# Performance work log

Hardware: AMD Instinct MI355X
Metric: run time of the kernel (lower is better)

The kernel has to match this reference:

```python
import jax, jax.numpy as jnp
import numpy as np

NH = 8       # attention_maps
DK = 256     # key_dimension
DV = 256     # value_dimension
KS = 3       # kernel_size
PAD = (KS - 1) // 2


def _conv(x, w, b, stride, pad):
    y = jax.lax.conv_general_dilated(
        x, w, (stride, stride), [(pad, pad), (pad, pad)],
        dimension_numbers=('NCHW', 'OIHW', 'NCHW'))
    return y + b[None, :, None, None]


def _rel_to_abs(x):
    # x: (B, M, L, 2L-1) -> (B, M, L, L) via the skewing/padding trick
    B, M, L, _ = x.shape
    x = jnp.pad(x, ((0, 0), (0, 0), (0, 0), (0, 1)))          # (B,M,L,2L)
    x = x.reshape(B, M, 2 * L * L)
    x = jnp.pad(x, ((0, 0), (0, 0), (0, L - 1)))
    x = x.reshape(B, M, L + 1, 2 * L - 1)
    return x[:, :, :L, L - 1:]


def _rel_logits_1d(q, kr, H, W, nh, axis):
    # q: (B, nh, H, W, dkh); kr: (2W-1, dkh)
    B = q.shape[0]
    rl = jnp.einsum('bhxyd,md->bhxym', q, kr)                 # (B,nh,H,W,2W-1)
    rl = rl.reshape(B, nh * H, W, 2 * W - 1)
    rl = _rel_to_abs(rl).reshape(B, nh, H, W, W)
    rl = jnp.broadcast_to(rl[:, :, :, None], (B, nh, H, H, W, W))
    if axis == 'x':
        rl = jnp.transpose(rl, (0, 1, 2, 4, 3, 5))
    else:
        # faithful to original torch code (incl. its no-op transpose bug):
        # transpose(4,5) then transpose(3,5) == permutation (0,1,2,4,5,3)
        rl = jnp.transpose(rl, (0, 1, 2, 4, 5, 3))
    return rl.reshape(B, nh, H * W, H * W)


def setup_inputs() -> dict:
    key = jax.random.key(0)
    ks = jax.random.split(key, 10)
    B, Cin, H, W = 4, 128, 32, 32
    Cout = 512
    dkh = DK // NH
    sc = 0.05
    return {
        'x': jax.random.normal(ks[0], (B, Cin, H, W), jnp.float32),
        'conv_w': jax.random.normal(ks[1], (Cout - DV, Cin, KS, KS), jnp.float32) * sc,
        'conv_b': jax.random.normal(ks[2], (Cout - DV,), jnp.float32) * sc,
        'qkv_w': jax.random.normal(ks[3], (2 * DK + DV, Cin, KS, KS), jnp.float32) * sc,
        'qkv_b': jax.random.normal(ks[4], (2 * DK + DV,), jnp.float32) * sc,
        'att_w': jax.random.normal(ks[5], (DV, DV, 1, 1), jnp.float32) * sc,
        'att_b': jax.random.normal(ks[6], (DV,), jnp.float32) * sc,
        'kr_x': jax.random.normal(ks[7], (2 * W - 1, dkh), jnp.float32),
        'kr_y': jax.random.normal(ks[8], (2 * H - 1, dkh), jnp.float32),
    }


def reference(x, conv_w, conv_b, qkv_w, qkv_b, att_w, att_b, kr_x, kr_y):
    B = x.shape[0]
    conv_out = _conv(x, conv_w, conv_b, 1, PAD)               # (B, Cout-DV, H, W)
    H, W = conv_out.shape[2], conv_out.shape[3]
    dkh, dvh = DK // NH, DV // NH

    qkv = _conv(x, qkv_w, qkv_b, 1, PAD)                      # (B, 2DK+DV, H, W)
    q, k, v = jnp.split(qkv, [DK, 2 * DK], axis=1)
    q = q.reshape(B, NH, dkh, H, W) * (dkh ** -0.5)
    k = k.reshape(B, NH, dkh, H, W)
    v = v.reshape(B, NH, dvh, H, W)

    fq = q.reshape(B, NH, dkh, H * W)
    fk = k.reshape(B, NH, dkh, H * W)
    fv = v.reshape(B, NH, dvh, H * W)

    logits = jnp.einsum('bhdi,bhdj->bhij', fq, fk)            # (B,NH,HW,HW)

    # relative logits (scaled q, matching torch which scales before this)
    q_t = jnp.transpose(q, (0, 1, 3, 4, 2))                   # (B,NH,H,W,dkh)
    rel_x = _rel_logits_1d(q_t, kr_x, H, W, NH, 'x')
    rel_y = _rel_logits_1d(jnp.transpose(q_t, (0, 1, 3, 2, 4)), kr_y, W, H, NH, 'y')
    logits = logits + rel_y + rel_x

    weights = jax.nn.softmax(logits, axis=-1)
    att = jnp.einsum('bhij,bhdj->bhid', weights, fv)          # (B,NH,HW,dvh)
    # faithful raw reshape as in torch (no transpose before reshape)
    att = att.reshape(B, NH, dvh, H, W).reshape(B, DV, H, W)
    att = _conv(att, att_w, att_b, 1, 0)
    return jnp.concatenate([conv_out, att], axis=1)
```

## Files before the change

kernel.cpp:

```cpp
#include <hip/hip_runtime.h>
#include <hip/hip_bf16.h>
#include <math.h>

#define BN 4
#define CIN 128
#define HH 32
#define WW 32
#define HWP 1024
#define NHEAD 8

typedef __attribute__((ext_vector_type(8))) short s8v;
typedef __attribute__((ext_vector_type(4))) float f32x4;

__global__ __launch_bounds__(256) void prep_all(
    const float* __restrict__ x,
    const float* __restrict__ conv_w, const float* __restrict__ qkv_w,
    const float* __restrict__ att_w,
    const float* __restrict__ kr_x, const float* __restrict__ kr_y,
    __hip_bfloat16* __restrict__ xT, __hip_bfloat16* __restrict__ Wb,
    __hip_bfloat16* __restrict__ Wab, __hip_bfloat16* __restrict__ krb)
{
    const int bid = blockIdx.x;
    const int tid = threadIdx.x;

    if (bid < 4608) {
        int g = bid * 256 + tid;
        int co = g / 1152;
        int k = g - co * 1152;
        int kk = k >> 7, ci = k & 127;
        float v;
        if (co < 256) v = conv_w[((size_t)(co * 128 + ci) * 9) + kk];
        else          v = qkv_w[((size_t)((co - 256) * 128 + ci) * 9) + kk];
        Wb[(size_t)co * 1152 + k] = __float2bfloat16(v);
    } else if (bid < 4744) {
        __shared__ float xs[CIN][33];
        int rel = bid - 4608;
        int yy = rel >> 2;
        int b = rel & 3;
        const bool inner = (yy >= 1 && yy <= 32);
        if (inner) {
            for (int idx = tid; idx < CIN * 32; idx += 256) {
                int ci = idx >> 5, xx = idx & 31;
                xs[ci][xx] = x[((size_t)(b * CIN + ci) * HH + (yy - 1)) * WW + xx];
            }
        }
        __syncthreads();
        for (int idx = tid; idx < 34 * 128; idx += 256) {
            int xx = idx >> 7, ci = idx & 127;
            float v = 0.f;
            if (inner && xx >= 1 && xx <= 32) v = xs[ci][xx - 1];
            xT[((size_t)(b * 34 + yy) * 34 + xx) * 128 + ci] = __float2bfloat16(v);
        }
    } else if (bid < 5000) {
        int g = (bid - 4744) * 256 + tid;
        Wab[g] = __float2bfloat16(att_w[g]);
    } else {
        for (int idx = tid; idx < 2 * 64 * 32; idx += 256) {
            int axis = idx >> 11;
            int col = (idx >> 5) & 63;
            int d = idx & 31;
            float v = 0.f;
            if (col < 63) v = axis ? kr_y[col * 32 + d] : kr_x[col * 32 + d];
            krb[idx] = __float2bfloat16(v);
        }
    }
}

__global__ __launch_bounds__(256) void conv_gemm(
    const __hip_bfloat16* __restrict__ Wb, const __hip_bfloat16* __restrict__ xT,
    const float* __restrict__ conv_b, const float* __restrict__ qkv_b,
    float* __restrict__ out,
    __hip_bfloat16* __restrict__ qbf, __hip_bfloat16* __restrict__ kbf,
    __hip_bfloat16* __restrict__ vtb)
{
    __shared__ __align__(16) __hip_bfloat16 As[128 * 128];
    __shared__ __align__(16) __hip_bfloat16 Bs[128 * 128];

    const int tid = threadIdx.x;
    const int wv = tid >> 6;
    const int lane = tid & 63;
    const int n16 = lane & 15;
    const int quad = lane >> 4;
    const int co0 = blockIdx.x * 128;
    const int y0 = blockIdx.y * 4;
    const int b = blockIdx.z;
    const int mh = wv >> 1, nh = wv & 1;

    const int rbase = tid >> 4;
    const int hh = tid & 15;
    const int swz = (hh ^ rbase) * 8;
    const __hip_bfloat16* aGbase = Wb + (size_t)(co0 + rbase) * 1152 + hh * 8;

    f32x4 acc[4][4];
#pragma unroll
    for (int i = 0; i < 4; ++i)
#pragma unroll
        for (int j = 0; j < 4; ++j) acc[i][j] = (f32x4){0.f, 0.f, 0.f, 0.f};

    s8v ra[8], rb[8];

    auto load_tile = [&](int kk, s8v* la, s8v* lb) {
        const int ky = kk / 3, kx = kk - ky * 3;
#pragma unroll
        for (int i = 0; i < 8; ++i)
            la[i] = *reinterpret_cast<const s8v*>(aGbase + (size_t)(16 * i) * 1152 + kk * 128);
#pragma unroll
        for (int i = 0; i < 8; ++i) {
            int p = rbase + 16 * i;
            int row = y0 + (p >> 5) + ky;
            int xx = (p & 31) + kx;
            lb[i] = *reinterpret_cast<const s8v*>(
                xT + ((size_t)(b * 34 + row) * 34 + xx) * 128 + hh * 8);
        }
    };

    load_tile(0, ra, rb);

    for (int s = 0; s < 9; ++s) {
        __syncthreads();
#pragma unroll
        for (int i = 0; i < 8; ++i) {
            *reinterpret_cast<s8v*>(&As[(rbase + 16 * i) * 128 + swz]) = ra[i];
            *reinterpret_cast<s8v*>(&Bs[(rbase + 16 * i) * 128 + swz]) = rb[i];
        }
        __syncthreads();
        if (s < 8) load_tile(s + 1, ra, rb);

#pragma unroll
        for (int ksub = 0; ksub < 4; ++ksub) {
            const int chunk = ((ksub * 4 + quad) ^ n16) * 8;
            s8v af[4], bfr[4];
#pragma unroll
            for (int mt = 0; mt < 4; ++mt)
                af[mt] = *reinterpret_cast<const s8v*>(&As[(mh * 64 + mt * 16 + n16) * 128 + chunk]);
#pragma unroll
            for (int nt = 0; nt < 4; ++nt)
                bfr[nt] = *reinterpret_cast<const s8v*>(&Bs[(nh * 64 + nt * 16 + n16) * 128 + chunk]);
#pragma unroll
            for (int mt = 0; mt < 4; ++mt)
#pragma unroll
                for (int nt = 0; nt < 4; ++nt)
                    acc[mt][nt] = __builtin_amdgcn_mfma_f32_16x16x32_bf16(af[mt], bfr[nt], acc[mt][nt], 0, 0, 0);
        }
    }

    const int coBase = co0 + mh * 64;
    const int pixBase = y0 * 32 + nh * 64;
    const int seg = coBase >> 8;

    if (seg == 0) {
#pragma unroll
        for (int mt = 0; mt < 4; ++mt)
#pragma unroll
            for (int r = 0; r < 4; ++r) {
                int co = coBase + mt * 16 + quad * 4 + r;
                float bias = conv_b[co];
                float* op = out + (size_t)(b * 512 + co) * HWP + pixBase;
#pragma unroll
                for (int nt = 0; nt < 4; ++nt)
                    op[nt * 16 + n16] = acc[mt][nt][r] + bias;
            }
    } else if (seg == 1) {
        const float scale = 0.17677669529663687f;
#pragma unroll
        for (int mt = 0; mt < 4; ++mt)
#pragma unroll
            for (int r = 0; r < 4; ++r) {
                int c2 = coBase - 256 + mt * 16 + quad * 4 + r;
                float bias = qkv_b[c2];
                int h = c2 >> 5, d = c2 & 31;
                int bh = b * NHEAD + h;
#pragma unroll
                for (int nt = 0; nt < 4; ++nt) {
                    int pix = pixBase + nt * 16 + n16;
                    qbf[((size_t)bh * HWP + pix) * 32 + d] =
                        __float2bfloat16((acc[mt][nt][r] + bias) * scale);
                }
            }
    } else if (seg == 2) {
#pragma unroll
        for (int mt = 0; mt < 4; ++mt)
#pragma unroll
            for (int r = 0; r < 4; ++r) {
                int c2 = coBase - 512 + mt * 16 + quad * 4 + r;
                float bias = qkv_b[c2 + 256];
                int h = c2 >> 5, d = c2 & 31;
                int bh = b * NHEAD + h;
#pragma unroll
                for (int nt = 0; nt < 4; ++nt) {
                    int pix = pixBase + nt * 16 + n16;
                    kbf[((size_t)bh * HWP + pix) * 32 + d] =
                        __float2bfloat16(acc[mt][nt][r] + bias);
                }
            }
    } else {
#pragma unroll
        for (int mt = 0; mt < 4; ++mt)
#pragma unroll
            for (int r = 0; r < 4; ++r) {
                int c2 = coBase - 768 + mt * 16 + quad * 4 + r;
                float bias = qkv_b[c2 + 512];
                int h = c2 >> 5, d = c2 & 31;
                int bh = b * NHEAD + h;
                __hip_bfloat16* vp = vtb + ((size_t)bh * 32 + d) * HWP + pixBase;
#pragma unroll
                for (int nt = 0; nt < 4; ++nt)
                    vp[nt * 16 + n16] = __float2bfloat16(acc[mt][nt][r] + bias);
            }
    }
}

__global__ __launch_bounds__(256) void attn_kernel(
    const __hip_bfloat16* __restrict__ qbf, const __hip_bfloat16* __restrict__ kbf,
    const __hip_bfloat16* __restrict__ vtb, const __hip_bfloat16* __restrict__ krb,
    __hip_bfloat16* __restrict__ attc)
{
    __shared__ __align__(16) float QrX[4][16][68];
    __shared__ __align__(16) float QrY[4][16][68];
    __shared__ __align__(16) __hip_bfloat16 Pb[4][16][40];

    const int tid = threadIdx.x;
    const int wv = tid >> 6;
    const int lane = tid & 63;
    const int n16 = lane & 15;
    const int quad = lane >> 4;
    const int bh = blockIdx.x;
    const int i0 = (blockIdx.y * 4 + wv) * 16;
    const int xi0 = i0 & 31;
    const int yi0 = i0 >> 5;

    s8v aq = *reinterpret_cast<const s8v*>(
        qbf + ((size_t)bh * HWP + i0 + n16) * 32 + quad * 8);
    s8v aqT = *reinterpret_cast<const s8v*>(
        qbf + ((size_t)bh * HWP + (xi0 + n16) * 32 + yi0) * 32 + quad * 8);

#pragma unroll
    for (int t = 0; t < 4; ++t) {
        s8v bx = *reinterpret_cast<const s8v*>(krb + ((size_t)(t * 16 + n16)) * 32 + quad * 8);
        s8v by = *reinterpret_cast<const s8v*>(krb + ((size_t)(64 + t * 16 + n16)) * 32 + quad * 8);
        f32x4 cx = {0.f, 0.f, 0.f, 0.f}, cy = {0.f, 0.f, 0.f, 0.f};
        cx = __builtin_amdgcn_mfma_f32_16x16x32_bf16(aq, bx, cx, 0, 0, 0);
        cy = __builtin_amdgcn_mfma_f32_16x16x32_bf16(aqT, by, cy, 0, 0, 0);
#pragma unroll
        for (int r = 0; r < 4; ++r) {
            QrX[wv][quad * 4 + r][t * 16 + n16] = cx[r];
            QrY[wv][quad * 4 + r][t * 16 + n16] = cy[r];
        }
    }

    float rx0[4], rx1[4];
    int rybase[4];
#pragma unroll
    for (int r = 0; r < 4; ++r) {
        int xi = xi0 + quad * 4 + r;
        rx0[r] = QrX[wv][quad * 4 + r][n16 + 31 - xi];
        rx1[r] = QrX[wv][quad * 4 + r][n16 + 47 - xi];
        rybase[r] = 31 - xi;
    }

    float lsum[4] = {0.f, 0.f, 0.f, 0.f};
    f32x4 O0 = {0.f, 0.f, 0.f, 0.f}, O1 = {0.f, 0.f, 0.f, 0.f};

    const __hip_bfloat16* kbase = kbf + (size_t)bh * HWP * 32;
    const __hip_bfloat16* vbase = vtb + (size_t)bh * 32 * HWP;

    s8v bk0 = *reinterpret_cast<const s8v*>(kbase + ((size_t)n16 * 32 + quad * 8));
    s8v bk1 = *reinterpret_cast<const s8v*>(kbase + ((size_t)(16 + n16) * 32 + quad * 8));
    s8v bv0 = *reinterpret_cast<const s8v*>(vbase + ((size_t)n16 * HWP + quad * 8));
    s8v bv1 = *reinterpret_cast<const s8v*>(vbase + ((size_t)(n16 + 16) * HWP + quad * 8));

    for (int jt = 0; jt < 32; ++jt) {
        s8v cbk0 = bk0, cbk1 = bk1, cbv0 = bv0, cbv1 = bv1;
        if (jt < 31) {
            const int jn = (jt + 1) * 32;
            bk0 = *reinterpret_cast<const s8v*>(kbase + ((size_t)(jn + n16) * 32 + quad * 8));
            bk1 = *reinterpret_cast<const s8v*>(kbase + ((size_t)(jn + 16 + n16) * 32 + quad * 8));
            bv0 = *reinterpret_cast<const s8v*>(vbase + ((size_t)n16 * HWP + jn + quad * 8));
            bv1 = *reinterpret_cast<const s8v*>(vbase + ((size_t)(n16 + 16) * HWP + jn + quad * 8));
        }

        f32x4 s0 = {0.f, 0.f, 0.f, 0.f}, s1 = {0.f, 0.f, 0.f, 0.f};
        s0 = __builtin_amdgcn_mfma_f32_16x16x32_bf16(aq, cbk0, s0, 0, 0, 0);
        s1 = __builtin_amdgcn_mfma_f32_16x16x32_bf16(aq, cbk1, s1, 0, 0, 0);

#pragma unroll
        for (int r = 0; r < 4; ++r) {
            float ryv = QrY[wv][quad * 4 + r][jt + rybase[r]];
            float p0 = __expf(s0[r] + rx0[r] + ryv);
            float p1 = __expf(s1[r] + rx1[r] + ryv);
            lsum[r] += p0 + p1;
            Pb[wv][quad * 4 + r][n16]      = __float2bfloat16(p0);
            Pb[wv][quad * 4 + r][n16 + 16] = __float2bfloat16(p1);
        }
        s8v pA = *reinterpret_cast<const s8v*>(&Pb[wv][n16][quad * 8]);
        O0 = __builtin_amdgcn_mfma_f32_16x16x32_bf16(pA, cbv0, O0, 0, 0, 0);
        O1 = __builtin_amdgcn_mfma_f32_16x16x32_bf16(pA, cbv1, O1, 0, 0, 0);
    }

    const int b = bh >> 3, h = bh & 7;
#pragma unroll
    for (int r = 0; r < 4; ++r) {
        float l = lsum[r];
        l += __shfl_xor(l, 1);
        l += __shfl_xor(l, 2);
        l += __shfl_xor(l, 4);
        l += __shfl_xor(l, 8);
        float inv = 1.0f / l;
        int i = i0 + quad * 4 + r;
        int yi = i >> 5, xi = i & 31;
        __hip_bfloat16* op = attc + ((size_t)(b * 256 + h * 32 + yi) * 32 + xi) * 32;
        op[n16] = __float2bfloat16(O0[r] * inv);
        op[n16 + 16] = __float2bfloat16(O1[r] * inv);
    }
}

__global__ __launch_bounds__(256) void conv1x1_gemm(
    const __hip_bfloat16* __restrict__ Wab, const __hip_bfloat16* __restrict__ attc,
    const float* __restrict__ att_b, float* __restrict__ out)
{
    __shared__ __align__(16) __hip_bfloat16 Ls[64][264];

    const int tid = threadIdx.x;
    const int wv = tid >> 6;
    const int lane = tid & 63;
    const int n16 = lane & 15;
    const int quad = lane >> 4;
    const int o0 = blockIdx.x * 64;
    const int p0 = blockIdx.y * 64;
    const int b = blockIdx.z;
    const int oW = o0 + (wv >> 1) * 32;
    const int pL = (wv & 1) * 32;

#pragma unroll
    for (int pass = 0; pass < 8; ++pass) {
        int ch = pass * 32 + (tid >> 3);
        int pg = (tid & 7) * 8;
        s8v v = *reinterpret_cast<const s8v*>(
            attc + ((size_t)(b * 256 + ch) * HWP) + p0 + pg);
#pragma unroll
        for (int j = 0; j < 8; ++j)
            Ls[pg + j][ch] = ((const __hip_bfloat16*)&v)[j];
    }
    __syncthreads();

    f32x4 acc[2][2];
#pragma unroll
    for (int i = 0; i < 2; ++i)
#pragma unroll
        for (int j = 0; j < 2; ++j) acc[i][j] = (f32x4){0.f, 0.f, 0.f, 0.f};

#pragma unroll
    for (int ks = 0; ks < 8; ++ks) {
        const int c0 = ks * 32 + quad * 8;
        s8v a0 = *reinterpret_cast<const s8v*>(Wab + (size_t)(oW + n16) * 256 + c0);
        s8v a1 = *reinterpret_cast<const s8v*>(Wab + (size_t)(oW + 16 + n16) * 256 + c0);
        s8v b0 = *reinterpret_cast<const s8v*>(&Ls[pL + n16][c0]);
        s8v b1 = *reinterpret_cast<const s8v*>(&Ls[pL + 16 + n16][c0]);
        acc[0][0] = __builtin_amdgcn_mfma_f32_16x16x32_bf16(a0, b0, acc[0][0], 0, 0, 0);
        acc[0][1] = __builtin_amdgcn_mfma_f32_16x16x32_bf16(a0, b1, acc[0][1], 0, 0, 0);
        acc[1][0] = __builtin_amdgcn_mfma_f32_16x16x32_bf16(a1, b0, acc[1][0], 0, 0, 0);
        acc[1][1] = __builtin_amdgcn_mfma_f32_16x16x32_bf16(a1, b1, acc[1][1], 0, 0, 0);
    }

#pragma unroll
    for (int mt = 0; mt < 2; ++mt)
#pragma unroll
        for (int r = 0; r < 4; ++r) {
            int o = oW + mt * 16 + quad * 4 + r;
            float bias = att_b[o];
            float* op = out + ((size_t)(b * 512 + 256 + o)) * HWP;
#pragma unroll
            for (int nt = 0; nt < 2; ++nt)
                op[p0 + pL + nt * 16 + n16] = acc[mt][nt][r] + bias;
        }
}

extern "C" void kernel_launch(void* const* d_in, const int* in_sizes, int n_in,
                              void* d_out, int out_size, void* d_ws, size_t ws_size,
                              hipStream_t stream) {
    const float* x      = (const float*)d_in[0];
    const float* conv_w = (const float*)d_in[1];
    const float* conv_b = (const float*)d_in[2];
    const float* qkv_w  = (const float*)d_in[3];
    const float* qkv_b  = (const float*)d_in[4];
    const float* att_w  = (const float*)d_in[5];
    const float* att_b  = (const float*)d_in[6];
    const float* kr_x   = (const float*)d_in[7];
    const float* kr_y   = (const float*)d_in[8];
    float* out = (float*)d_out;

    char* base = (char*)d_ws;
    const size_t MB = 1u << 20;
    __hip_bfloat16* qbf  = (__hip_bfloat16*)(base + 0 * MB);
    __hip_bfloat16* kbf  = (__hip_bfloat16*)(base + 2 * MB);
    __hip_bfloat16* vtb  = (__hip_bfloat16*)(base + 4 * MB);
    __hip_bfloat16* xT   = (__hip_bfloat16*)(base + 6 * MB);
    __hip_bfloat16* Wb   = (__hip_bfloat16*)(base + 8 * MB);
    __hip_bfloat16* attc = (__hip_bfloat16*)(base + 11 * MB);
    __hip_bfloat16* Wab  = (__hip_bfloat16*)(base + 13 * MB);
    __hip_bfloat16* krb  = (__hip_bfloat16*)(base + 14 * MB);

    prep_all<<<dim3(5001), 256, 0, stream>>>(
        x, conv_w, qkv_w, att_w, kr_x, kr_y, xT, Wb, Wab, krb);
    conv_gemm<<<dim3(8, 8, 4), 256, 0, stream>>>(
        Wb, xT, conv_b, qkv_b, out, qbf, kbf, vtb);
    attn_kernel<<<dim3(32, 16), 256, 0, stream>>>(qbf, kbf, vtb, krb, attc);
    conv1x1_gemm<<<dim3(4, 16, 4), 256, 0, stream>>>(Wab, attc, att_b, out);
}
```

Baseline: 140.1 us.

## Coalesce weight prep via LDS and halve conv GEMM pixel tile for more blocks

The weight-conversion part of prep_all now has each block read 8 output channels contiguously, transpose them through shared memory into the k-major bf16 layout, and write them out coalesced. This replaces the strided gather over 4608 blocks and cuts the prep grid to 329 blocks. The att_w conversion now uses float4 loads. conv_gemm tiles 128 channels by 64 pixels instead of 128 by 128, doubling the grid to 512 flattened blocks for better CU occupancy, at the cost of less reuse of A tiles per block.

```diff
diff --git a/kernel.cpp b/kernel.cpp
--- a/kernel.cpp
+++ b/kernel.cpp
@@ -23,18 +23,30 @@
     const int bid = blockIdx.x;
     const int tid = threadIdx.x;
 
-    if (bid < 4608) {
-        int g = bid * 256 + tid;
-        int co = g / 1152;
-        int k = g - co * 1152;
-        int kk = k >> 7, ci = k & 127;
-        float v;
-        if (co < 256) v = conv_w[((size_t)(co * 128 + ci) * 9) + kk];
-        else          v = qkv_w[((size_t)((co - 256) * 128 + ci) * 9) + kk];
-        Wb[(size_t)co * 1152 + k] = __float2bfloat16(v);
-    } else if (bid < 4744) {
+    if (bid < 128) {
+        __shared__ __hip_bfloat16 Ws[8 * 1152];
+        const int co0 = bid * 8;
+        const float* src = (co0 < 256) ? (conv_w + (size_t)co0 * 1152)
+                                       : (qkv_w + (size_t)(co0 - 256) * 1152);
+#pragma unroll
+        for (int pass = 0; pass < 36; ++pass) {
+            int idx = pass * 256 + tid;
+            float v = src[idx];
+            int col = idx / 1152;
+            int r = idx - col * 1152;
+            int ci = r / 9;
+            int kk = r - ci * 9;
+            Ws[col * 1152 + kk * 128 + ci] = __float2bfloat16(v);
+        }
+        __syncthreads();
+        const unsigned* Lu = (const unsigned*)Ws;
+        unsigned* Ou = (unsigned*)(Wb + (size_t)co0 * 1152);
+#pragma unroll
+        for (int pass = 0; pass < 18; ++pass)
+            Ou[pass * 256 + tid] = Lu[pass * 256 + tid];
+    } else if (bid < 264) {
         __shared__ float xs[CIN][33];
-        int rel = bid - 4608;
+        int rel = bid - 128;
         int yy = rel >> 2;
         int b = rel & 3;
         const bool inner = (yy >= 1 && yy <= 32);
@@ -51,9 +63,13 @@
             if (inner && xx >= 1 && xx <= 32) v = xs[ci][xx - 1];
             xT[((size_t)(b * 34 + yy) * 34 + xx) * 128 + ci] = __float2bfloat16(v);
         }
-    } else if (bid < 5000) {
-        int g = (bid - 4744) * 256 + tid;
-        Wab[g] = __float2bfloat16(att_w[g]);
+    } else if (bid < 328) {
+        int g = ((bid - 264) * 256 + tid) * 4;
+        float4 v = *(const float4*)(att_w + g);
+        Wab[g + 0] = __float2bfloat16(v.x);
+        Wab[g + 1] = __float2bfloat16(v.y);
+        Wab[g + 2] = __float2bfloat16(v.z);
+        Wab[g + 3] = __float2bfloat16(v.w);
     } else {
         for (int idx = tid; idx < 2 * 64 * 32; idx += 256) {
             int axis = idx >> 11;
@@ -74,78 +90,80 @@
     __hip_bfloat16* __restrict__ vtb)
 {
     __shared__ __align__(16) __hip_bfloat16 As[128 * 128];
-    __shared__ __align__(16) __hip_bfloat16 Bs[128 * 128];
+    __shared__ __align__(16) __hip_bfloat16 Bs[64 * 128];
 
     const int tid = threadIdx.x;
     const int wv = tid >> 6;
     const int lane = tid & 63;
     const int n16 = lane & 15;
     const int quad = lane >> 4;
-    const int co0 = blockIdx.x * 128;
-    const int y0 = blockIdx.y * 4;
-    const int b = blockIdx.z;
+    const int bid = blockIdx.x;
+    const int ph = bid & 1;
+    const int b = (bid >> 1) & 3;
+    const int yt = (bid >> 3) & 7;
+    const int ct = bid >> 6;
+    const int co0 = ct * 128;
+    const int pixBase = yt * 128 + ph * 64;
+    const int row0 = pixBase >> 5;
     const int mh = wv >> 1, nh = wv & 1;
-
     const int rbase = tid >> 4;
     const int hh = tid & 15;
     const int swz = (hh ^ rbase) * 8;
     const __hip_bfloat16* aGbase = Wb + (size_t)(co0 + rbase) * 1152 + hh * 8;
 
-    f32x4 acc[4][4];
+    f32x4 acc[4][2];
 #pragma unroll
     for (int i = 0; i < 4; ++i)
 #pragma unroll
-        for (int j = 0; j < 4; ++j) acc[i][j] = (f32x4){0.f, 0.f, 0.f, 0.f};
-
-    s8v ra[8], rb[8];
-
+        for (int j = 0; j < 2; ++j) acc[i][j] = (f32x4){0.f, 0.f, 0.f, 0.f};
+
+    s8v ra[8], rb2[4];
     auto load_tile = [&](int kk, s8v* la, s8v* lb) {
         const int ky = kk / 3, kx = kk - ky * 3;
 #pragma unroll
         for (int i = 0; i < 8; ++i)
             la[i] = *reinterpret_cast<const s8v*>(aGbase + (size_t)(16 * i) * 1152 + kk * 128);
 #pragma unroll
-        for (int i = 0; i < 8; ++i) {
+        for (int i = 0; i < 4; ++i) {
             int p = rbase + 16 * i;
-            int row = y0 + (p >> 5) + ky;
-            int xx = (p & 31) + kx;
             lb[i] = *reinterpret_cast<const s8v*>(
-                xT + ((size_t)(b * 34 + row) * 34 + xx) * 128 + hh * 8);
+                xT + ((size_t)(b * 34 + row0 + (p >> 5) + ky) * 34 + (p & 31) + kx) * 128 + hh * 8);
         }
     };
 
-    load_tile(0, ra, rb);
+    load_tile(0, ra, rb2);
 
     for (int s = 0; s < 9; ++s) {
         __syncthreads();
 #pragma unroll
-        for (int i = 0; i < 8; ++i) {
+        for (int i = 0; i < 8; ++i)
             *reinterpret_cast<s8v*>(&As[(rbase + 16 * i) * 128 + swz]) = ra[i];
-            *reinterpret_cast<s8v*>(&Bs[(rbase + 16 * i) * 128 + swz]) = rb[i];
-        }
+#pragma unroll
+        for (int i = 0; i < 4; ++i)
+            *reinterpret_cast<s8v*>(&Bs[(rbase + 16 * i) * 128 + swz]) = rb2[i];
         __syncthreads();
-        if (s < 8) load_tile(s + 1, ra, rb);
+        if (s < 8) load_tile(s + 1, ra, rb2);
 
 #pragma unroll
         for (int ksub = 0; ksub < 4; ++ksub) {
             const int chunk = ((ksub * 4 + quad) ^ n16) * 8;
-            s8v af[4], bfr[4];
+            s8v af[4], bfr[2];
 #pragma unroll
             for (int mt = 0; mt < 4; ++mt)
                 af[mt] = *reinterpret_cast<const s8v*>(&As[(mh * 64 + mt * 16 + n16) * 128 + chunk]);
 #pragma unroll
-            for (int nt = 0; nt < 4; ++nt)
-                bfr[nt] = *reinterpret_cast<const s8v*>(&Bs[(nh * 64 + nt * 16 + n16) * 128 + chunk]);
+            for (int nt = 0; nt < 2; ++nt)
+                bfr[nt] = *reinterpret_cast<const s8v*>(&Bs[(nh * 32 + nt * 16 + n16) * 128 + chunk]);
 #pragma unroll
             for (int mt = 0; mt < 4; ++mt)
 #pragma unroll
-                for (int nt = 0; nt < 4; ++nt)
+                for (int nt = 0; nt < 2; ++nt)
                     acc[mt][nt] = __builtin_amdgcn_mfma_f32_16x16x32_bf16(af[mt], bfr[nt], acc[mt][nt], 0, 0, 0);
         }
     }
 
     const int coBase = co0 + mh * 64;
-    const int pixBase = y0 * 32 + nh * 64;
+    const int pixW = pixBase + nh * 32;
     const int seg = coBase >> 8;
 
     if (seg == 0) {
@@ -155,9 +173,9 @@
             for (int r = 0; r < 4; ++r) {
                 int co = coBase + mt * 16 + quad * 4 + r;
                 float bias = conv_b[co];
-                float* op = out + (size_t)(b * 512 + co) * HWP + pixBase;
-#pragma unroll
-                for (int nt = 0; nt < 4; ++nt)
+                float* op = out + (size_t)(b * 512 + co) * HWP + pixW;
+#pragma unroll
+                for (int nt = 0; nt < 2; ++nt)
                     op[nt * 16 + n16] = acc[mt][nt][r] + bias;
             }
     } else if (seg == 1) {
@@ -171,8 +189,8 @@
                 int h = c2 >> 5, d = c2 & 31;
                 int bh = b * NHEAD + h;
 #pragma unroll
-                for (int nt = 0; nt < 4; ++nt) {
-                    int pix = pixBase + nt * 16 + n16;
+                for (int nt = 0; nt < 2; ++nt) {
+                    int pix = pixW + nt * 16 + n16;
                     qbf[((size_t)bh * HWP + pix) * 32 + d] =
                         __float2bfloat16((acc[mt][nt][r] + bias) * scale);
                 }
@@ -187,8 +205,8 @@
                 int h = c2 >> 5, d = c2 & 31;
                 int bh = b * NHEAD + h;
 #pragma unroll
-                for (int nt = 0; nt < 4; ++nt) {
-                    int pix = pixBase + nt * 16 + n16;
+                for (int nt = 0; nt < 2; ++nt) {
+                    int pix = pixW + nt * 16 + n16;
                     kbf[((size_t)bh * HWP + pix) * 32 + d] =
                         __float2bfloat16(acc[mt][nt][r] + bias);
                 }
@@ -202,9 +220,9 @@
                 float bias = qkv_b[c2 + 512];
                 int h = c2 >> 5, d = c2 & 31;
                 int bh = b * NHEAD + h;
-                __hip_bfloat16* vp = vtb + ((size_t)bh * 32 + d) * HWP + pixBase;
-#pragma unroll
-                for (int nt = 0; nt < 4; ++nt)
+                __hip_bfloat16* vp = vtb + ((size_t)bh * 32 + d) * HWP + pixW;
+#pragma unroll
+                for (int nt = 0; nt < 2; ++nt)
                     vp[nt * 16 + n16] = __float2bfloat16(acc[mt][nt][r] + bias);
             }
     }
@@ -400,9 +418,9 @@
     __hip_bfloat16* Wab  = (__hip_bfloat16*)(base + 13 * MB);
     __hip_bfloat16* krb  = (__hip_bfloat16*)(base + 14 * MB);
 
-    prep_all<<<dim3(5001), 256, 0, stream>>>(
+    prep_all<<<dim3(329), 256, 0, stream>>>(
         x, conv_w, qkv_w, att_w, kr_x, kr_y, xT, Wb, Wab, krb);
-    conv_gemm<<<dim3(8, 8, 4), 256, 0, stream>>>(
+    conv_gemm<<<dim3(512), 256, 0, stream>>>(
         Wb, xT, conv_b, qkv_b, out, qbf, kbf, vtb);
     attn_kernel<<<dim3(32, 16), 256, 0, stream>>>(qbf, kbf, vtb, krb, attc);
     conv1x1_gemm<<<dim3(4, 16, 4), 256, 0, stream>>>(Wab, attc, att_b, out);
```

Result: faster. 134.0 us (-4.4%).
